# Performance work log

Hardware: AMD Instinct MI355X
Metric: run time of the kernel (lower is better)

The kernel has to match this reference:

```python
import jax, jax.numpy as jnp
import numpy as np

N = 8192
IN_FEATS = 256
D = IN_FEATS // 4  # 64, bottleneck dim
HID = 64           # MLP hidden_dim
K_MAX = 9
K_EC = 20
SLOPE = 0.01       # torch LeakyReLU default


def _leaky(x):
    return jnp.where(x >= 0, x, SLOPE * x)


def _knn_idx(f, k):
    # f: [N, d]; returns [N, k] indices of k nearest (incl. self, dist 0), ascending distance
    sq = jnp.sum(f * f, axis=1)
    dist = sq[:, None] + sq[None, :] - 2.0 * (f @ f.T)  # [N, N]
    _, idx = jax.lax.top_k(-dist, k)
    return idx


def _edge_conv(f, idx, Wt, bt, Wp, bp, W1, b1, W2, b2):
    # f: [N, d]; idx: [N, k] neighbor (src) indices; dst is the row node.
    x_nb = f[idx]                                   # [N, k, d] gather of src feats
    theta = (f[:, None, :] - x_nb) @ Wt.T + bt      # v_sub_u -> theta Linear
    phi = f @ Wp.T + bp                             # [N, d]
    z = phi[:, None, :] + theta                     # [N, k, d]
    # MLP(hidden=64, 2 layers, leaky_relu, activation_first=True)
    z = _leaky(z) @ W1.T + b1
    z = _leaky(z) @ W2.T + b2
    return jnp.max(z, axis=1)                       # max aggregation per dst


def _lin_init(key, out_dim, in_dim):
    k1, k2 = jax.random.split(key)
    bound = 1.0 / np.sqrt(in_dim)
    W = jax.random.uniform(k1, (out_dim, in_dim), jnp.float32, -bound, bound)
    b = jax.random.uniform(k2, (out_dim,), jnp.float32, -bound, bound)
    return W, b


def setup_inputs() -> dict:
    key = jax.random.key(0)
    keys = jax.random.split(key, 12)
    inp = {"feature": jax.random.normal(keys[0], (N, IN_FEATS), jnp.float32)}
    inp["Wb"], inp["bb"] = _lin_init(keys[1], D, IN_FEATS)
    inp["Wt1"], inp["bt1"] = _lin_init(keys[2], D, D)
    inp["Wp1"], inp["bp1"] = _lin_init(keys[3], D, D)
    inp["Wm1a"], inp["bm1a"] = _lin_init(keys[4], HID, D)
    inp["Wm1b"], inp["bm1b"] = _lin_init(keys[5], D, HID)
    inp["Wt2"], inp["bt2"] = _lin_init(keys[6], D, D)
    inp["Wp2"], inp["bp2"] = _lin_init(keys[7], D, D)
    inp["Wm2a"], inp["bm2a"] = _lin_init(keys[8], HID, D)
    inp["Wm2b"], inp["bm2b"] = _lin_init(keys[9], D, HID)
    inp["Wl"], inp["bl"] = _lin_init(keys[10], IN_FEATS, 3 * D)
    return inp


def reference(feature, Wb, bb, Wt1, bt1, Wp1, bp1, Wm1a, bm1a, Wm1b, bm1b,
              Wt2, bt2, Wp2, bp2, Wm2a, bm2a, Wm2b, bm2b, Wl, bl):
    f = feature @ Wb.T + bb                          # bottleneck [N, D]
    # KNN indices are non-differentiable (torch topk indices) -> stop_gradient
    idx40 = _knn_idx(jax.lax.stop_gradient(f), K_EC * 2)  # 40-NN, ascending distance
    idx9 = idx40[:, :K_MAX]
    idx20 = idx40[:, :K_EC]            # dilation 1
    idx20_d2 = idx40[:, ::2]           # dilation 2: every 2nd of 40-NN
    h_max = jnp.max(f[idx9], axis=1)   # copy_u + max over 9-NN
    h1 = _edge_conv(f, idx20, Wt1, bt1, Wp1, bp1, Wm1a, bm1a, Wm1b, bm1b)
    h2 = _edge_conv(f, idx20_d2, Wt2, bt2, Wp2, bp2, Wm2a, bm2a, Wm2b, bm2b)
    h = jnp.concatenate([h1, h2, h_max], axis=1) @ Wl.T + bl
    return h + feature                 # residual
```

## Files before the change

### kernel.cpp

```cpp
#include <hip/hip_runtime.h>
#include <math.h>

#define NPT   8192
#define FIN   256
#define DD    64
#define KSEL  48
#define SSEG  320

#define LEAKY(x) (((x) >= 0.f) ? (x) : 0.01f*(x))

using short8v = __attribute__((ext_vector_type(8))) short;
using f32x4   = __attribute__((ext_vector_type(4))) float;

__device__ inline unsigned short f2bf(float x) {
  union { float f; unsigned u; } v; v.f = x;
  unsigned r = v.u + 0x7fff + ((v.u >> 16) & 1);
  return (unsigned short)(r >> 16);
}
__device__ inline float bf2f(unsigned short h) {
  union { unsigned u; float f; } v; v.u = ((unsigned)h) << 16; return v.f;
}
__device__ inline unsigned key_of(float f) {
  unsigned u = __float_as_uint(f);
  return (u & 0x80000000u) ? ~u : (u | 0x80000000u);
}
__device__ inline float key_inv(unsigned k) {
  unsigned u = (k >> 31) ? (k ^ 0x80000000u) : ~k;
  return __uint_as_float(u);
}

__global__ void k0_prep(const float* __restrict__ Wl, const float* __restrict__ Wb,
                        const float* __restrict__ Wt1, const float* __restrict__ Wp1,
                        const float* __restrict__ Wt2, const float* __restrict__ Wp2,
                        float* __restrict__ WlT, float* __restrict__ WbT,
                        float* __restrict__ WtT1, float* __restrict__ WpT1,
                        float* __restrict__ WtT2, float* __restrict__ WpT2)
{
  const int b = blockIdx.x, t = threadIdx.x;
  if (b < 192) {
    WlT[b*256 + t] = Wl[t*192 + b];
  } else if (b < 256) {
    int j = (b - 192)*4 + (t >> 6), o = t & 63;
    WbT[j*64 + o] = Wb[o*256 + j];
  } else {
    int m = b - 256;
    const float* src = (m==0) ? Wt1 : (m==1) ? Wp1 : (m==2) ? Wt2 : Wp2;
    float*       dst = (m==0) ? WtT1: (m==1) ? WpT1: (m==2) ? WtT2: WpT2;
    #pragma unroll
    for (int i = 0; i < 16; ++i) {
      int idx = t + 256*i, r = idx >> 6, c = idx & 63;
      dst[c*64 + r] = src[r*64 + c];
    }
  }
}

__global__ __launch_bounds__(256) void k1_precompute(
    const float* __restrict__ feature, const float* __restrict__ WbT, const float* __restrict__ bb,
    const float* __restrict__ WtT1, const float* __restrict__ bt1,
    const float* __restrict__ WpT1, const float* __restrict__ bp1,
    const float* __restrict__ WtT2, const float* __restrict__ bt2,
    const float* __restrict__ WpT2, const float* __restrict__ bp2,
    double* __restrict__ f64d, double* __restrict__ sq64,
    float* __restrict__ f32v, float* __restrict__ sqf,
    float* __restrict__ u1, float* __restrict__ c1,
    float* __restrict__ u2, float* __restrict__ c2)
{
  __shared__ float f_s[4*64];
  const int w = threadIdx.x >> 6, l = threadIdx.x & 63;
  const int i = blockIdx.x*4 + w;
  const float* frow = feature + i*FIN;
  double a0 = (double)bb[l], a1 = 0.0, a2 = 0.0, a3 = 0.0;
  #pragma unroll 2
  for (int j = 0; j < FIN; j += 4) {
    float4 fv = *(const float4*)&frow[j];
    a0 += (double)fv.x * (double)WbT[(j+0)*64 + l];
    a1 += (double)fv.y * (double)WbT[(j+1)*64 + l];
    a2 += (double)fv.z * (double)WbT[(j+2)*64 + l];
    a3 += (double)fv.w * (double)WbT[(j+3)*64 + l];
  }
  double facc = (a0 + a1) + (a2 + a3);
  f64d[i*DD + l] = facc;
  float f32 = (float)facc;
  f32v[i*DD + l] = f32;
  double s = facc*facc;
  #pragma unroll
  for (int off = 32; off; off >>= 1) s += __shfl_xor(s, off);
  if (l == 0) { sq64[i] = s; sqf[i] = (float)s; }
  f_s[w*64 + l] = f32;
  float au1 = 0.f, ap1 = 0.f, au2 = 0.f, ap2 = 0.f;
  for (int e = 0; e < DD; ++e) {
    float fe = f_s[w*64 + e];
    au1 += fe * WtT1[e*64 + l];
    ap1 += fe * WpT1[e*64 + l];
    au2 += fe * WtT2[e*64 + l];
    ap2 += fe * WpT2[e*64 + l];
  }
  u1[i*DD+l] = au1;
  c1[i*DD+l] = ap1 + bp1[l] + au1 + bt1[l];
  u2[i*DD+l] = au2;
  c2[i*DD+l] = ap2 + bp2[l] + au2 + bt2[l];
}

__global__ __launch_bounds__(256) void k1b_frag(
    const float* __restrict__ f32v,
    unsigned short* __restrict__ Saf, unsigned short* __restrict__ Sbf)
{
  const int w = threadIdx.x >> 6, l = threadIdx.x & 63;
  const int task = blockIdx.x*4 + w;
  const int tile = task / 6, ks = task % 6;
  const int row  = tile*16 + (l & 15);
  const int inner = (ks & 1)*32 + ((l >> 4) << 3);
  union { unsigned short u[8]; short8v v; } pa, pb;
  #pragma unroll
  for (int j = 0; j < 8; ++j) {
    float x = f32v[row*64 + inner + j];
    unsigned short hi = f2bf(x);
    unsigned short lo = f2bf(x - bf2f(hi));
    pa.u[j] = (ks < 4) ? hi : lo;
    pb.u[j] = (ks < 2) ? hi : ((ks < 4) ? lo : hi);
  }
  size_t off = ((size_t)(tile*6 + ks)*64 + l)*8;
  *(short8v*)&Saf[off] = pa.v;
  *(short8v*)&Sbf[off] = pb.v;
}

__global__ __launch_bounds__(256) void k1c_wfrag(
    const float* __restrict__ Wm1a, const float* __restrict__ Wm1b,
    const float* __restrict__ Wm2a, const float* __restrict__ Wm2b,
    unsigned short* __restrict__ F1a, unsigned short* __restrict__ F1b,
    unsigned short* __restrict__ F2a, unsigned short* __restrict__ F2b)
{
  const int w = threadIdx.x >> 6, l = threadIdx.x & 63;
  const int task = blockIdx.x*4 + w;
  const int which = task / 24, rem = task % 24;
  const int nt = rem / 6, ks = rem % 6;
  const float* W = (which==0) ? Wm1a : (which==1) ? Wm1b : (which==2) ? Wm2a : Wm2b;
  unsigned short* F = (which==0) ? F1a : (which==1) ? F1b : (which==2) ? F2a : F2b;
  const int row = nt*16 + (l & 15);
  const int inner = (ks & 1)*32 + ((l >> 4) << 3);
  union { unsigned short u[8]; short8v v; } p;
  #pragma unroll
  for (int j = 0; j < 8; ++j) {
    float x = W[row*64 + inner + j];
    unsigned short hi = f2bf(x);
    unsigned short lo = f2bf(x - bf2f(hi));
    p.u[j] = (ks < 2) ? hi : ((ks < 4) ? lo : hi);
  }
  *(short8v*)&F[((size_t)(nt*6 + ks)*64 + l)*8] = p.v;
}

#define MFMA_PAIR6(ACC, AF, BF)                                                  \
  ACC = __builtin_amdgcn_mfma_f32_16x16x32_bf16(AF[0], BF[0], ACC, 0, 0, 0);     \
  ACC = __builtin_amdgcn_mfma_f32_16x16x32_bf16(AF[1], BF[1], ACC, 0, 0, 0);     \
  ACC = __builtin_amdgcn_mfma_f32_16x16x32_bf16(AF[0], BF[2], ACC, 0, 0, 0);     \
  ACC = __builtin_amdgcn_mfma_f32_16x16x32_bf16(AF[1], BF[3], ACC, 0, 0, 0);     \
  ACC = __builtin_amdgcn_mfma_f32_16x16x32_bf16(AF[2], BF[0], ACC, 0, 0, 0);     \
  ACC = __builtin_amdgcn_mfma_f32_16x16x32_bf16(AF[3], BF[1], ACC, 0, 0, 0);

__global__ __launch_bounds__(512) void k2a_sample(
    const unsigned short* __restrict__ Saf,
    const unsigned short* __restrict__ Sbf,
    const float* __restrict__ sqf,
    float* __restrict__ sampD)
{
  const int t = threadIdx.x, w = t >> 6, l = t & 63;
  const int qb = blockIdx.x >> 1, sh = blockIdx.x & 1;
  const int qbase = qb * 32;
  short8v afr[2][4];
  #pragma unroll
  for (int mt = 0; mt < 2; ++mt) {
    const size_t b = (size_t)(qb*2 + mt)*6;
    afr[mt][0] = *(const short8v*)&Saf[((b+0)*64 + l)*8];
    afr[mt][1] = *(const short8v*)&Saf[((b+1)*64 + l)*8];
    afr[mt][2] = *(const short8v*)&Saf[((b+4)*64 + l)*8];
    afr[mt][3] = *(const short8v*)&Saf[((b+5)*64 + l)*8];
  }
  const int ncol = w*16 + (l & 15);
  for (int sl = 0; sl < 4; ++sl) {
    const int s = sh*4 + sl;
    const int cb = s*8;
    const int jbase = cb*128;
    short8v bfr[4];
    {
      const size_t b = (size_t)(cb*8 + w)*6;
      #pragma unroll
      for (int k = 0; k < 4; ++k)
        bfr[k] = *(const short8v*)&Sbf[((b+k)*64 + l)*8];
    }
    const float sc = sqf[jbase + ncol];
    f32x4 acc0 = {0.f,0.f,0.f,0.f}, acc1 = {0.f,0.f,0.f,0.f};
    MFMA_PAIR6(acc0, afr[0], bfr);
    MFMA_PAIR6(acc1, afr[1], bfr);
    #pragma unroll
    for (int r = 0; r < 4; ++r) {
      const int q0 = qbase + 0*16 + (l >> 4)*4 + r;
      const int q1 = qbase + 1*16 + (l >> 4)*4 + r;
      sampD[(size_t)q0*1024 + s*128 + ncol] = sc - 2.0f*acc0[r];
      sampD[(size_t)q1*1024 + s*128 + ncol] = sc - 2.0f*acc1[r];
    }
  }
}

__global__ __launch_bounds__(256) void k2t_threshold(
    const float* __restrict__ sampD, float* __restrict__ Tq)
{
  const int w = threadIdx.x >> 6, l = threadIdx.x & 63;
  const int q = blockIdx.x*4 + w;
  unsigned ku[16];
  #pragma unroll
  for (int k = 0; k < 16; ++k)
    ku[k] = key_of(sampD[(size_t)q*1024 + k*64 + l]);
  unsigned prefix = 0; int need = 41;
  for (int b = 31; b >= 0; --b) {
    unsigned p2 = prefix << 1;
    int c = 0;
    #pragma unroll
    for (int k = 0; k < 16; ++k) c += ((ku[k] >> b) == p2);
    #pragma unroll
    for (int off = 32; off; off >>= 1) c += __shfl_xor(c, off);
    if (c >= need) prefix = p2; else { prefix = p2 | 1u; need -= c; }
  }
  if (l == 0) Tq[q] = key_inv(prefix);
}

__global__ __launch_bounds__(512) void k2f_filter(
    const unsigned short* __restrict__ Saf,
    const unsigned short* __restrict__ Sbf,
    const float* __restrict__ sqf,
    const float* __restrict__ Tq,
    int* __restrict__ cnt_g,
    float* __restrict__ survD, int* __restrict__ survI)
{
  __shared__ int cnt_sh[32];
  const int t = threadIdx.x, w = t >> 6, l = t & 63;
  const int qb = blockIdx.x >> 1, half = blockIdx.x & 1;
  const int qbase = qb * 32;
  if (t < 32) cnt_sh[t] = 0;
  short8v afr[2][4];
  float Tr[2][4]; int qloc[2][4];
  #pragma unroll
  for (int mt = 0; mt < 2; ++mt) {
    const size_t b = (size_t)(qb*2 + mt)*6;
    afr[mt][0] = *(const short8v*)&Saf[((b+0)*64 + l)*8];
    afr[mt][1] = *(const short8v*)&Saf[((b+1)*64 + l)*8];
    afr[mt][2] = *(const short8v*)&Saf[((b+4)*64 + l)*8];
    afr[mt][3] = *(const short8v*)&Saf[((b+5)*64 + l)*8];
    #pragma unroll
    for (int r = 0; r < 4; ++r) {
      qloc[mt][r] = mt*16 + (l >> 4)*4 + r;
      Tr[mt][r] = Tq[qbase + qloc[mt][r]];
    }
  }
  short8v bfr[4];
  {
    const size_t b = (size_t)(half*256 + w)*6;
    #pragma unroll
    for (int k = 0; k < 4; ++k)
      bfr[k] = *(const short8v*)&Sbf[((b+k)*64 + l)*8];
  }
  const int ncol = w*16 + (l & 15);
  __syncthreads();
  for (int cb = 0; cb < 32; ++cb) {
    const int jbase = half*4096 + cb*128;
    const float sc = sqf[jbase + ncol];
    f32x4 acc0 = {0.f,0.f,0.f,0.f}, acc1 = {0.f,0.f,0.f,0.f};
    MFMA_PAIR6(acc0, afr[0], bfr);
    MFMA_PAIR6(acc1, afr[1], bfr);
    if (cb < 31) {
      const size_t b = (size_t)(half*256 + (cb+1)*8 + w)*6;
      #pragma unroll
      for (int k = 0; k < 4; ++k)
        bfr[k] = *(const short8v*)&Sbf[((b+k)*64 + l)*8];
    }
    const int j = jbase + ncol;
    #pragma unroll
    for (int r = 0; r < 4; ++r) {
      float d0 = sc - 2.0f*acc0[r];
      if (d0 < Tr[0][r]) {
        int slot = atomicAdd(&cnt_sh[qloc[0][r]], 1);
        if (slot < SSEG) {
          size_t base = ((size_t)(qbase + qloc[0][r])*2 + half)*SSEG + slot;
          survD[base] = d0; survI[base] = j;
        }
      }
      float d1 = sc - 2.0f*acc1[r];
      if (d1 < Tr[1][r]) {
        int slot = atomicAdd(&cnt_sh[qloc[1][r]], 1);
        if (slot < SSEG) {
          size_t base = ((size_t)(qbase + qloc[1][r])*2 + half)*SSEG + slot;
          survD[base] = d1; survI[base] = j;
        }
      }
    }
  }
  __syncthreads();
  if (t < 32) cnt_g[(qbase + t)*2 + half] = cnt_sh[t];
}

__global__ __launch_bounds__(256) void k2s_select(
    const float* __restrict__ survD, const int* __restrict__ survI,
    const int* __restrict__ cnt_g, int* __restrict__ idx48)
{
  const int w = threadIdx.x >> 6, l = threadIdx.x & 63;
  const int node = blockIdx.x*4 + w;
  const int c0 = min(cnt_g[node*2 + 0], SSEG);
  const int c1 = min(cnt_g[node*2 + 1], SSEG);
  unsigned ku[10]; int iv[10];
  #pragma unroll
  for (int k = 0; k < 10; ++k) {
    int e = k*64 + l;
    int seg = (e >= SSEG);
    int off = e - seg*SSEG;
    bool v = off < (seg ? c1 : c0);
    size_t base = ((size_t)node*2 + seg)*SSEG + off;
    float d = v ? survD[base] : 0.f;
    iv[k] = v ? survI[base] : 0;
    ku[k] = v ? key_of(d) : 0xFFFFFFFFu;
  }
  unsigned prefix = 0; int need = KSEL;
  for (int b = 31; b >= 0; --b) {
    unsigned p2 = prefix << 1;
    int c = 0;
    #pragma unroll
    for (int k = 0; k < 10; ++k) c += ((ku[k] >> b) == p2);
    #pragma unroll
    for (int off = 32; off; off >>= 1) c += __shfl_xor(c, off);
    if (c >= need) prefix = p2; else { prefix = p2 | 1u; need -= c; }
  }
  const unsigned long long below = (1ull << l) - 1ull;
  int base = 0;
  #pragma unroll
  for (int k = 0; k < 10; ++k) {
    unsigned long long blt = __ballot(ku[k] < prefix);
    if (ku[k] < prefix) {
      int pos = base + __popcll(blt & below);
      idx48[(size_t)node*KSEL + pos] = iv[k];
    }
    base += __popcll(blt);
  }
  #pragma unroll
  for (int k = 0; k < 10; ++k) {
    unsigned long long beq = __ballot(ku[k] == prefix);
    if (ku[k] == prefix) {
      int pos = base + __popcll(beq & below);
      if (pos < KSEL) idx48[(size_t)node*KSEL + pos] = iv[k];
    }
    base += __popcll(beq);
  }
}

__global__ __launch_bounds__(256) void k2r_rerank(
    const double* __restrict__ f64d, const double* __restrict__ sq64,
    const int* __restrict__ idx48, int* __restrict__ idx40)
{
  __shared__ double part[KSEL][4];
  __shared__ double dist_sh[KSEL];
  __shared__ int    cand_sh[KSEL];
  const int t = threadIdx.x;
  const int node = blockIdx.x;
  if (t < KSEL) cand_sh[t] = idx48[(size_t)node*KSEL + t];
  __syncthreads();
  if (t < 192) {
    int c = t >> 2, qt = t & 3;
    int cand = cand_sh[c];
    const double* fi = f64d + (size_t)node*DD + qt*16;
    const double* fc = f64d + (size_t)cand*DD + qt*16;
    double a0 = 0.0, a1 = 0.0;
    #pragma unroll
    for (int d = 0; d < 16; d += 2) { a0 += fi[d]*fc[d]; a1 += fi[d+1]*fc[d+1]; }
    part[c][qt] = a0 + a1;
  }
  __syncthreads();
  if (t < KSEL) {
    int cand = cand_sh[t];
    dist_sh[t] = sq64[node] + sq64[cand]
               - 2.0*(part[t][0] + part[t][1] + part[t][2] + part[t][3]);
  }
  __syncthreads();
  if (t < KSEL) {
    double dm = dist_sh[t]; int cand = cand_sh[t];
    int rank = 0;
    for (int j = 0; j < KSEL; ++j) {
      double dj = dist_sh[j];
      int    ij = cand_sh[j];
      rank += (dj < dm) || (dj == dm && ij < cand);
    }
    if (rank < 40) idx40[(size_t)node*40 + rank] = cand;
  }
}

#define MFMA6(ACC, AF, W0, W1, W2, W3)                                          \
  ACC = __builtin_amdgcn_mfma_f32_16x16x32_bf16(AF[0], W0, ACC, 0, 0, 0);       \
  ACC = __builtin_amdgcn_mfma_f32_16x16x32_bf16(AF[1], W1, ACC, 0, 0, 0);       \
  ACC = __builtin_amdgcn_mfma_f32_16x16x32_bf16(AF[0], W2, ACC, 0, 0, 0);       \
  ACC = __builtin_amdgcn_mfma_f32_16x16x32_bf16(AF[1], W3, ACC, 0, 0, 0);       \
  ACC = __builtin_amdgcn_mfma_f32_16x16x32_bf16(AF[2], W0, ACC, 0, 0, 0);       \
  ACC = __builtin_amdgcn_mfma_f32_16x16x32_bf16(AF[3], W1, ACC, 0, 0, 0);

__global__ __launch_bounds__(256) void k3_edgeconv(
    const float* __restrict__ f32v,
    const float* __restrict__ u1, const float* __restrict__ c1,
    const float* __restrict__ u2, const float* __restrict__ c2,
    const unsigned short* __restrict__ F1a, const unsigned short* __restrict__ F1b,
    const unsigned short* __restrict__ F2a, const unsigned short* __restrict__ F2b,
    const float* __restrict__ bm1a, const float* __restrict__ bm1b,
    const float* __restrict__ bm2a, const float* __restrict__ bm2b,
    const int* __restrict__ idx40, float* __restrict__ hout)
{
  __shared__ __align__(16) unsigned au32[32*66];
  __shared__ float red_s[2*64];
  __shared__ int idx_sh[40];
  const int t = threadIdx.x, i = blockIdx.x;
  const int w = t >> 6, l = t & 63;
  const int mt = w >> 1;
  const int nb0 = (w & 1)*2;
  const int row16 = l & 15;
  const int q8 = (l >> 4) << 3;
  if (t < 40) idx_sh[t] = idx40[i*40 + t];
  __syncthreads();

  for (int conv = 0; conv < 2; ++conv) {
    const float* u_g = conv ? u2 : u1;
    const float* c_g = conv ? c2 : c1;
    const unsigned short* WfA = conv ? F2a : F1a;
    const unsigned short* WfB = conv ? F2b : F1b;
    const float* bav = conv ? bm2a : bm1a;
    const float* bbv = conv ? bm2b : bm1b;

    const int row = mt*16 + row16;
    const bool valid = row < 20;
    const int nb = valid ? idx_sh[conv ? 2*row : row] : idx_sh[0];
    short8v afr[4];
    {
      const float* up = u_g + (size_t)nb*DD;
      const float* cp = c_g + (size_t)i*DD;
      float4 ua = *(const float4*)&up[q8];
      float4 ub = *(const float4*)&up[q8 + 4];
      float4 uc = *(const float4*)&up[32 + q8];
      float4 ud = *(const float4*)&up[32 + q8 + 4];
      float4 ca = *(const float4*)&cp[q8];
      float4 cb2 = *(const float4*)&cp[q8 + 4];
      float4 cc = *(const float4*)&cp[32 + q8];
      float4 cd = *(const float4*)&cp[32 + q8 + 4];
      float z0[8], z1[8];
      z0[0]=ca.x-ua.x;  z0[1]=ca.y-ua.y;  z0[2]=ca.z-ua.z;  z0[3]=ca.w-ua.w;
      z0[4]=cb2.x-ub.x; z0[5]=cb2.y-ub.y; z0[6]=cb2.z-ub.z; z0[7]=cb2.w-ub.w;
      z1[0]=cc.x-uc.x;  z1[1]=cc.y-uc.y;  z1[2]=cc.z-uc.z;  z1[3]=cc.w-uc.w;
      z1[4]=cd.x-ud.x;  z1[5]=cd.y-ud.y;  z1[6]=cd.z-ud.z;  z1[7]=cd.w-ud.w;
      union { unsigned short us[8]; short8v v; } fh0, fh1, fl0, fl1;
      #pragma unroll
      for (int j = 0; j < 8; ++j) {
        float x0 = valid ? LEAKY(z0[j]) : 0.f;
        float x1 = valid ? LEAKY(z1[j]) : 0.f;
        unsigned short h0 = f2bf(x0);
        unsigned short h1 = f2bf(x1);
        fh0.us[j] = h0; fl0.us[j] = f2bf(x0 - bf2f(h0));
        fh1.us[j] = h1; fl1.us[j] = f2bf(x1 - bf2f(h1));
      }
      afr[0] = fh0.v; afr[1] = fh1.v; afr[2] = fl0.v; afr[3] = fl1.v;
    }
    f32x4 acc0 = {0.f,0.f,0.f,0.f}, acc1 = {0.f,0.f,0.f,0.f};
    {
      const unsigned short* p0 = WfA + ((size_t)(nb0+0)*6*64)*8;
      const unsigned short* p1 = WfA + ((size_t)(nb0+1)*6*64)*8;
      short8v w00 = *(const short8v*)&p0[(0*64+l)*8];
      short8v w01 = *(const short8v*)&p0[(1*64+l)*8];
      short8v w02 = *(const short8v*)&p0[(2*64+l)*8];
      short8v w03 = *(const short8v*)&p0[(3*64+l)*8];
      short8v w10 = *(const short8v*)&p1[(0*64+l)*8];
      short8v w11 = *(const short8v*)&p1[(1*64+l)*8];
      short8v w12 = *(const short8v*)&p1[(2*64+l)*8];
      short8v w13 = *(const short8v*)&p1[(3*64+l)*8];
      MFMA6(acc0, afr, w00, w01, w02, w03);
      MFMA6(acc1, afr, w10, w11, w12, w13);
    }
    {
      const int c0 = (nb0+0)*16 + row16, c1i = (nb0+1)*16 + row16;
      const float ba0 = bav[c0], ba1 = bav[c1i];
      #pragma unroll
      for (int r = 0; r < 4; ++r) {
        const int arow = mt*16 + (l >> 4)*4 + r;
        float v0 = acc0[r] + ba0; v0 = LEAKY(v0);
        float v1 = acc1[r] + ba1; v1 = LEAKY(v1);
        unsigned short h0 = f2bf(v0), h1 = f2bf(v1);
        unsigned lo0 = f2bf(v0 - bf2f(h0));
        unsigned lo1 = f2bf(v1 - bf2f(h1));
        au32[arow*66 + c0]  = (unsigned)h0 | (lo0 << 16);
        au32[arow*66 + c1i] = (unsigned)h1 | (lo1 << 16);
      }
    }
    __syncthreads();
    short8v bfr[4];
    {
      const int base = (mt*16 + row16)*66 + q8;
      union { unsigned u[4]; short8v v; } bh0, bh1, bl0, bl1;
      #pragma unroll
      for (int p = 0; p < 4; ++p) {
        uint2 lo2 = *(const uint2*)&au32[base + 2*p];
        uint2 hi2 = *(const uint2*)&au32[base + 32 + 2*p];
        bh0.u[p] = (lo2.x & 0xFFFFu) | (lo2.y << 16);
        bl0.u[p] = (lo2.x >> 16)     | (lo2.y & 0xFFFF0000u);
        bh1.u[p] = (hi2.x & 0xFFFFu) | (hi2.y << 16);
        bl1.u[p] = (hi2.x >> 16)     | (hi2.y & 0xFFFF0000u);
      }
      bfr[0] = bh0.v; bfr[1] = bh1.v; bfr[2] = bl0.v; bfr[3] = bl1.v;
    }
    f32x4 bacc0 = {0.f,0.f,0.f,0.f}, bacc1 = {0.f,0.f,0.f,0.f};
    {
      const unsigned short* p0 = WfB + ((size_t)(nb0+0)*6*64)*8;
      const unsigned short* p1 = WfB + ((size_t)(nb0+1)*6*64)*8;
      short8v w00 = *(const short8v*)&p0[(0*64+l)*8];
      short8v w01 = *(const short8v*)&p0[(1*64+l)*8];
      short8v w02 = *(const short8v*)&p0[(2*64+l)*8];
      short8v w03 = *(const short8v*)&p0[(3*64+l)*8];
      short8v w10 = *(const short8v*)&p1[(0*64+l)*8];
      short8v w11 = *(const short8v*)&p1[(1*64+l)*8];
      short8v w12 = *(const short8v*)&p1[(2*64+l)*8];
      short8v w13 = *(const short8v*)&p1[(3*64+l)*8];
      MFMA6(bacc0, bfr, w00, w01, w02, w03);
      MFMA6(bacc1, bfr, w10, w11, w12, w13);
    }
    {
      const int c0 = (nb0+0)*16 + row16, c1i = (nb0+1)*16 + row16;
      const float bb0 = bbv[c0], bb1 = bbv[c1i];
      float m0 = -__builtin_inff(), m1 = -__builtin_inff();
      #pragma unroll
      for (int r = 0; r < 4; ++r) {
        const int arow = mt*16 + (l >> 4)*4 + r;
        if (arow < 20) {
          m0 = fmaxf(m0, bacc0[r] + bb0);
          m1 = fmaxf(m1, bacc1[r] + bb1);
        }
      }
      m0 = fmaxf(m0, __shfl_xor(m0, 16)); m0 = fmaxf(m0, __shfl_xor(m0, 32));
      m1 = fmaxf(m1, __shfl_xor(m1, 16)); m1 = fmaxf(m1, __shfl_xor(m1, 32));
      if ((l >> 4) == 0) {
        red_s[mt*64 + c0]  = m0;
        red_s[mt*64 + c1i] = m1;
      }
    }
    __syncthreads();
    if (t < 64) hout[i*192 + conv*64 + t] = fmaxf(red_s[t], red_s[64 + t]);
    __syncthreads();
  }
  if (t < 64) {
    float m = -__builtin_inff();
    #pragma unroll
    for (int k = 0; k < 9; ++k) m = fmaxf(m, f32v[idx_sh[k]*DD + t]);
    hout[i*192 + 128 + t] = m;
  }
}

__global__ __launch_bounds__(256) void k4_final(
    const float* __restrict__ hbuf, const float* __restrict__ WlT,
    const float* __restrict__ bl, const float* __restrict__ feature,
    float* __restrict__ out)
{
  __shared__ __align__(16) float h_sh[16*192];
  const int t = threadIdx.x;
  const int nbase = blockIdx.x * 16;
  #pragma unroll
  for (int r = 0; r < 3; ++r) {
    int flat = t + 256*r;
    int n = flat / 48, j4 = flat % 48;
    *(float4*)&h_sh[n*192 + 4*j4] = *(const float4*)&hbuf[(nbase+n)*192 + 4*j4];
  }
  __syncthreads();
  float acc[16];
  #pragma unroll
  for (int n = 0; n < 16; ++n) acc[n] = 0.f;
  for (int j4 = 0; j4 < 48; ++j4) {
    float w0 = WlT[(4*j4+0)*256 + t];
    float w1 = WlT[(4*j4+1)*256 + t];
    float w2 = WlT[(4*j4+2)*256 + t];
    float w3 = WlT[(4*j4+3)*256 + t];
    #pragma unroll
    for (int n = 0; n < 16; ++n) {
      float4 hv = *(const float4*)&h_sh[n*192 + 4*j4];
      acc[n] += hv.x*w0 + hv.y*w1 + hv.z*w2 + hv.w*w3;
    }
  }
  float blv = bl[t];
  #pragma unroll
  for (int n = 0; n < 16; ++n)
    out[(nbase+n)*256 + t] = acc[n] + blv + feature[(nbase+n)*256 + t];
}

extern "C" void kernel_launch(void* const* d_in, const int* in_sizes, int n_in,
                              void* d_out, int out_size, void* d_ws, size_t ws_size,
                              hipStream_t stream) {
  const float* feature = (const float*)d_in[0];
  const float* Wb   = (const float*)d_in[1];
  const float* bb   = (const float*)d_in[2];
  const float* Wt1  = (const float*)d_in[3];
  const float* bt1  = (const float*)d_in[4];
  const float* Wp1  = (const float*)d_in[5];
  const float* bp1  = (const float*)d_in[6];
  const float* Wm1a = (const float*)d_in[7];
  const float* bm1a = (const float*)d_in[8];
  const float* Wm1b = (const float*)d_in[9];
  const float* bm1b = (const float*)d_in[10];
  const float* Wt2  = (const float*)d_in[11];
  const float* bt2  = (const float*)d_in[12];
  const float* Wp2  = (const float*)d_in[13];
  const float* bp2  = (const float*)d_in[14];
  const float* Wm2a = (const float*)d_in[15];
  const float* bm2a = (const float*)d_in[16];
  const float* Wm2b = (const float*)d_in[17];
  const float* bm2b = (const float*)d_in[18];
  const float* Wl   = (const float*)d_in[19];
  const float* bl   = (const float*)d_in[20];
  float* out = (float*)d_out;

  char* ws = (char*)d_ws;
  double* f64d = (double*)(ws + 0);
  double* sq64 = (double*)(ws + 4194304);
  float*  f32v = (float*)(ws + 4259840);
  float*  sqf  = (float*)(ws + 6356992);
  float*  u1   = (float*)(ws + 6389760);
  float*  c1   = (float*)(ws + 8486912);
  float*  u2   = (float*)(ws + 10584064);
  float*  c2   = (float*)(ws + 12681216);
  int*    idx48= (int*)(ws + 14778368);
  int*    idx40= (int*)(ws + 16351232);
  float*  hbuf = (float*)(ws + 17661952);
  float*  WlT  = (float*)(ws + 23953408);
  unsigned short* Saf = (unsigned short*)(ws + 24150016);
  unsigned short* Sbf = (unsigned short*)(ws + 27295744);
  float*  WbT  = (float*)(ws + 30441472);
  float*  WtT1 = (float*)(ws + 30507008);
  float*  WpT1 = (float*)(ws + 30523392);
  float*  WtT2 = (float*)(ws + 30539776);
  float*  WpT2 = (float*)(ws + 30556160);
  unsigned short* F1a = (unsigned short*)(ws + 30572544);
  unsigned short* F1b = (unsigned short*)(ws + 30597120);
  unsigned short* F2a = (unsigned short*)(ws + 30621696);
  unsigned short* F2b = (unsigned short*)(ws + 30646272);
  float*  Tq   = (float*)(ws + 30670848);
  int*    cnt_g= (int*)(ws + 30703616);
  float*  survD= (float*)(ws + 30769152);
  int*    survI= (int*)(ws + 51740672);
  float*  sampD= (float*)(ws + 30769152);

  hipLaunchKernelGGL(k0_prep, dim3(260), dim3(256), 0, stream,
                     Wl, Wb, Wt1, Wp1, Wt2, Wp2, WlT, WbT, WtT1, WpT1, WtT2, WpT2);
  hipLaunchKernelGGL(k1c_wfrag, dim3(24), dim3(256), 0, stream,
                     Wm1a, Wm1b, Wm2a, Wm2b, F1a, F1b, F2a, F2b);
  hipLaunchKernelGGL(k1_precompute, dim3(2048), dim3(256), 0, stream,
                     feature, WbT, bb, WtT1, bt1, WpT1, bp1, WtT2, bt2, WpT2, bp2,
                     f64d, sq64, f32v, sqf, u1, c1, u2, c2);
  hipLaunchKernelGGL(k1b_frag, dim3(768), dim3(256), 0, stream, f32v, Saf, Sbf);
  hipLaunchKernelGGL(k2a_sample, dim3(512), dim3(512), 0, stream, Saf, Sbf, sqf, sampD);
  hipLaunchKernelGGL(k2t_threshold, dim3(2048), dim3(256), 0, stream, sampD, Tq);
  hipLaunchKernelGGL(k2f_filter, dim3(512), dim3(512), 0, stream,
                     Saf, Sbf, sqf, Tq, cnt_g, survD, survI);
  hipLaunchKernelGGL(k2s_select, dim3(2048), dim3(256), 0, stream, survD, survI, cnt_g, idx48);
  hipLaunchKernelGGL(k2r_rerank, dim3(8192), dim3(256), 0, stream, f64d, sq64, idx48, idx40);
  hipLaunchKernelGGL(k3_edgeconv, dim3(8192), dim3(256), 0, stream,
                     f32v, u1, c1, u2, c2, F1a, F1b, F2a, F2b,
                     bm1a, bm1b, bm2a, bm2b, idx40, hbuf);
  hipLaunchKernelGGL(k4_final, dim3(512), dim3(256), 0, stream, hbuf, WlT, bl, feature, out);
}
```

Baseline: 432.6 us.

## Drop split-bf16 MLP in edgeconv and process two nodes per block

The edgeconv MLP previously used a hi/lo bf16 split (six MFMAs per output tile) to approximate fp32 precision. It now uses plain bf16 operands (two MFMAs per tile), and each wave computes all four output column tiles. Each block now handles two destination nodes, halving the grid. The goal is to cut MFMA and conversion work and block launch overhead, at the cost of lower numerical precision in the MLP, which could threaten tolerance.

New measurement: 396.7 us. 1.09x faster.

```diff
diff --git a/kernel.cpp b/kernel.cpp
--- a/kernel.cpp
+++ b/kernel.cpp
@@ -389,14 +389,6 @@
   }
 }
 
-#define MFMA6(ACC, AF, W0, W1, W2, W3)                                          \
-  ACC = __builtin_amdgcn_mfma_f32_16x16x32_bf16(AF[0], W0, ACC, 0, 0, 0);       \
-  ACC = __builtin_amdgcn_mfma_f32_16x16x32_bf16(AF[1], W1, ACC, 0, 0, 0);       \
-  ACC = __builtin_amdgcn_mfma_f32_16x16x32_bf16(AF[0], W2, ACC, 0, 0, 0);       \
-  ACC = __builtin_amdgcn_mfma_f32_16x16x32_bf16(AF[1], W3, ACC, 0, 0, 0);       \
-  ACC = __builtin_amdgcn_mfma_f32_16x16x32_bf16(AF[2], W0, ACC, 0, 0, 0);       \
-  ACC = __builtin_amdgcn_mfma_f32_16x16x32_bf16(AF[3], W1, ACC, 0, 0, 0);
-
 __global__ __launch_bounds__(256) void k3_edgeconv(
     const float* __restrict__ f32v,
     const float* __restrict__ u1, const float* __restrict__ c1,
@@ -407,16 +399,16 @@
     const float* __restrict__ bm2a, const float* __restrict__ bm2b,
     const int* __restrict__ idx40, float* __restrict__ hout)
 {
-  __shared__ __align__(16) unsigned au32[32*66];
-  __shared__ float red_s[2*64];
-  __shared__ int idx_sh[40];
-  const int t = threadIdx.x, i = blockIdx.x;
+  __shared__ unsigned short au16[2][32*72];
+  __shared__ float red_s[2][2][64];
+  __shared__ int idx_sh[80];
+  const int t = threadIdx.x;
   const int w = t >> 6, l = t & 63;
-  const int mt = w >> 1;
-  const int nb0 = (w & 1)*2;
+  const int sub = w >> 1, mt = w & 1;
+  const int i = blockIdx.x*2 + sub;
   const int row16 = l & 15;
   const int q8 = (l >> 4) << 3;
-  if (t < 40) idx_sh[t] = idx40[i*40 + t];
+  if (t < 80) idx_sh[t] = idx40[(size_t)(blockIdx.x*2 + (t >= 40))*40 + (t >= 40 ? t - 40 : t)];
   __syncthreads();
 
   for (int conv = 0; conv < 2; ++conv) {
@@ -429,8 +421,8 @@
 
     const int row = mt*16 + row16;
     const bool valid = row < 20;
-    const int nb = valid ? idx_sh[conv ? 2*row : row] : idx_sh[0];
-    short8v afr[4];
+    const int nb = valid ? idx_sh[sub*40 + (conv ? 2*row : row)] : idx_sh[sub*40];
+    short8v fr0, fr1;
     {
       const float* up = u_g + (size_t)nb*DD;
       const float* cp = c_g + (size_t)i*DD;
@@ -439,115 +431,88 @@
       float4 uc = *(const float4*)&up[32 + q8];
       float4 ud = *(const float4*)&up[32 + q8 + 4];
       float4 ca = *(const float4*)&cp[q8];
-      float4 cb2 = *(const float4*)&cp[q8 + 4];
+      float4 cb = *(const float4*)&cp[q8 + 4];
       float4 cc = *(const float4*)&cp[32 + q8];
       float4 cd = *(const float4*)&cp[32 + q8 + 4];
-      float z0[8], z1[8];
-      z0[0]=ca.x-ua.x;  z0[1]=ca.y-ua.y;  z0[2]=ca.z-ua.z;  z0[3]=ca.w-ua.w;
-      z0[4]=cb2.x-ub.x; z0[5]=cb2.y-ub.y; z0[6]=cb2.z-ub.z; z0[7]=cb2.w-ub.w;
-      z1[0]=cc.x-uc.x;  z1[1]=cc.y-uc.y;  z1[2]=cc.z-uc.z;  z1[3]=cc.w-uc.w;
-      z1[4]=cd.x-ud.x;  z1[5]=cd.y-ud.y;  z1[6]=cd.z-ud.z;  z1[7]=cd.w-ud.w;
-      union { unsigned short us[8]; short8v v; } fh0, fh1, fl0, fl1;
+      float z0[8] = {ca.x-ua.x, ca.y-ua.y, ca.z-ua.z, ca.w-ua.w,
+                     cb.x-ub.x, cb.y-ub.y, cb.z-ub.z, cb.w-ub.w};
+      float z1[8] = {cc.x-uc.x, cc.y-uc.y, cc.z-uc.z, cc.w-uc.w,
+                     cd.x-ud.x, cd.y-ud.y, cd.z-ud.z, cd.w-ud.w};
+      union { unsigned short us[8]; short8v v; } h0, h1;
       #pragma unroll
       for (int j = 0; j < 8; ++j) {
         float x0 = valid ? LEAKY(z0[j]) : 0.f;
         float x1 = valid ? LEAKY(z1[j]) : 0.f;
-        unsigned short h0 = f2bf(x0);
-        unsigned short h1 = f2bf(x1);
-        fh0.us[j] = h0; fl0.us[j] = f2bf(x0 - bf2f(h0));
-        fh1.us[j] = h1; fl1.us[j] = f2bf(x1 - bf2f(h1));
+        h0.us[j] = f2bf(x0);
+        h1.us[j] = f2bf(x1);
       }
-      afr[0] = fh0.v; afr[1] = fh1.v; afr[2] = fl0.v; afr[3] = fl1.v;
-    }
-    f32x4 acc0 = {0.f,0.f,0.f,0.f}, acc1 = {0.f,0.f,0.f,0.f};
-    {
-      const unsigned short* p0 = WfA + ((size_t)(nb0+0)*6*64)*8;
-      const unsigned short* p1 = WfA + ((size_t)(nb0+1)*6*64)*8;
-      short8v w00 = *(const short8v*)&p0[(0*64+l)*8];
-      short8v w01 = *(const short8v*)&p0[(1*64+l)*8];
-      short8v w02 = *(const short8v*)&p0[(2*64+l)*8];
-      short8v w03 = *(const short8v*)&p0[(3*64+l)*8];
-      short8v w10 = *(const short8v*)&p1[(0*64+l)*8];
-      short8v w11 = *(const short8v*)&p1[(1*64+l)*8];
-      short8v w12 = *(const short8v*)&p1[(2*64+l)*8];
-      short8v w13 = *(const short8v*)&p1[(3*64+l)*8];
-      MFMA6(acc0, afr, w00, w01, w02, w03);
-      MFMA6(acc1, afr, w10, w11, w12, w13);
-    }
-    {
-      const int c0 = (nb0+0)*16 + row16, c1i = (nb0+1)*16 + row16;
-      const float ba0 = bav[c0], ba1 = bav[c1i];
+      fr0 = h0.v; fr1 = h1.v;
+    }
+    f32x4 acc[4] = {{0,0,0,0},{0,0,0,0},{0,0,0,0},{0,0,0,0}};
+    #pragma unroll
+    for (int nt = 0; nt < 4; ++nt) {
+      const unsigned short* p = WfA + (size_t)nt*6*64*8;
+      short8v w0 = *(const short8v*)&p[(0*64 + l)*8];
+      short8v w1 = *(const short8v*)&p[(1*64 + l)*8];
+      acc[nt] = __builtin_amdgcn_mfma_f32_16x16x32_bf16(fr0, w0, acc[nt], 0, 0, 0);
+      acc[nt] = __builtin_amdgcn_mfma_f32_16x16x32_bf16(fr1, w1, acc[nt], 0, 0, 0);
+    }
+    #pragma unroll
+    for (int nt = 0; nt < 4; ++nt) {
+      const int col = nt*16 + row16;
+      const float ba = bav[col];
       #pragma unroll
       for (int r = 0; r < 4; ++r) {
         const int arow = mt*16 + (l >> 4)*4 + r;
-        float v0 = acc0[r] + ba0; v0 = LEAKY(v0);
-        float v1 = acc1[r] + ba1; v1 = LEAKY(v1);
-        unsigned short h0 = f2bf(v0), h1 = f2bf(v1);
-        unsigned lo0 = f2bf(v0 - bf2f(h0));
-        unsigned lo1 = f2bf(v1 - bf2f(h1));
-        au32[arow*66 + c0]  = (unsigned)h0 | (lo0 << 16);
-        au32[arow*66 + c1i] = (unsigned)h1 | (lo1 << 16);
+        float v = acc[nt][r] + ba; v = LEAKY(v);
+        au16[sub][arow*72 + col] = f2bf(v);
       }
     }
     __syncthreads();
-    short8v bfr[4];
+    short8v g0, g1;
     {
-      const int base = (mt*16 + row16)*66 + q8;
-      union { unsigned u[4]; short8v v; } bh0, bh1, bl0, bl1;
-      #pragma unroll
-      for (int p = 0; p < 4; ++p) {
-        uint2 lo2 = *(const uint2*)&au32[base + 2*p];
-        uint2 hi2 = *(const uint2*)&au32[base + 32 + 2*p];
-        bh0.u[p] = (lo2.x & 0xFFFFu) | (lo2.y << 16);
-        bl0.u[p] = (lo2.x >> 16)     | (lo2.y & 0xFFFF0000u);
-        bh1.u[p] = (hi2.x & 0xFFFFu) | (hi2.y << 16);
-        bl1.u[p] = (hi2.x >> 16)     | (hi2.y & 0xFFFF0000u);
-      }
-      bfr[0] = bh0.v; bfr[1] = bh1.v; bfr[2] = bl0.v; bfr[3] = bl1.v;
-    }
-    f32x4 bacc0 = {0.f,0.f,0.f,0.f}, bacc1 = {0.f,0.f,0.f,0.f};
-    {
-      const unsigned short* p0 = WfB + ((size_t)(nb0+0)*6*64)*8;
-      const unsigned short* p1 = WfB + ((size_t)(nb0+1)*6*64)*8;
-      short8v w00 = *(const short8v*)&p0[(0*64+l)*8];
-      short8v w01 = *(const short8v*)&p0[(1*64+l)*8];
-      short8v w02 = *(const short8v*)&p0[(2*64+l)*8];
-      short8v w03 = *(const short8v*)&p0[(3*64+l)*8];
-      short8v w10 = *(const short8v*)&p1[(0*64+l)*8];
-      short8v w11 = *(const short8v*)&p1[(1*64+l)*8];
-      short8v w12 = *(const short8v*)&p1[(2*64+l)*8];
-      short8v w13 = *(const short8v*)&p1[(3*64+l)*8];
-      MFMA6(bacc0, bfr, w00, w01, w02, w03);
-      MFMA6(bacc1, bfr, w10, w11, w12, w13);
-    }
-    {
-      const int c0 = (nb0+0)*16 + row16, c1i = (nb0+1)*16 + row16;
-      const float bb0 = bbv[c0], bb1 = bbv[c1i];
-      float m0 = -__builtin_inff(), m1 = -__builtin_inff();
+      const unsigned short* base = &au16[sub][(mt*16 + row16)*72 + q8];
+      g0 = *(const short8v*)&base[0];
+      g1 = *(const short8v*)&base[32];
+    }
+    f32x4 bacc[4] = {{0,0,0,0},{0,0,0,0},{0,0,0,0},{0,0,0,0}};
+    #pragma unroll
+    for (int nt = 0; nt < 4; ++nt) {
+      const unsigned short* p = WfB + (size_t)nt*6*64*8;
+      short8v w0 = *(const short8v*)&p[(0*64 + l)*8];
+      short8v w1 = *(const short8v*)&p[(1*64 + l)*8];
+      bacc[nt] = __builtin_amdgcn_mfma_f32_16x16x32_bf16(g0, w0, bacc[nt], 0, 0, 0);
+      bacc[nt] = __builtin_amdgcn_mfma_f32_16x16x32_bf16(g1, w1, bacc[nt], 0, 0, 0);
+    }
+    #pragma unroll
+    for (int nt = 0; nt < 4; ++nt) {
+      const int col = nt*16 + row16;
+      const float bb2 = bbv[col];
+      float m = -__builtin_inff();
       #pragma unroll
       for (int r = 0; r < 4; ++r) {
         const int arow = mt*16 + (l >> 4)*4 + r;
-        if (arow < 20) {
-          m0 = fmaxf(m0, bacc0[r] + bb0);
-          m1 = fmaxf(m1, bacc1[r] + bb1);
-        }
+        if (arow < 20) m = fmaxf(m, bacc[nt][r] + bb2);
       }
-      m0 = fmaxf(m0, __shfl_xor(m0, 16)); m0 = fmaxf(m0, __shfl_xor(m0, 32));
-      m1 = fmaxf(m1, __shfl_xor(m1, 16)); m1 = fmaxf(m1, __shfl_xor(m1, 32));
-      if ((l >> 4) == 0) {
-        red_s[mt*64 + c0]  = m0;
-        red_s[mt*64 + c1i] = m1;
-      }
+      m = fmaxf(m, __shfl_xor(m, 16));
+      m = fmaxf(m, __shfl_xor(m, 32));
+      if ((l >> 4) == 0) red_s[sub][mt][col] = m;
     }
     __syncthreads();
-    if (t < 64) hout[i*192 + conv*64 + t] = fmaxf(red_s[t], red_s[64 + t]);
+    if (t < 128) {
+      int s2 = t >> 6, col = t & 63;
+      hout[(size_t)(blockIdx.x*2 + s2)*192 + conv*64 + col] =
+          fmaxf(red_s[s2][0][col], red_s[s2][1][col]);
+    }
     __syncthreads();
   }
-  if (t < 64) {
+  if (t < 128) {
+    int s2 = t >> 6, col = t & 63;
     float m = -__builtin_inff();
     #pragma unroll
-    for (int k = 0; k < 9; ++k) m = fmaxf(m, f32v[idx_sh[k]*DD + t]);
-    hout[i*192 + 128 + t] = m;
+    for (int k = 0; k < 9; ++k)
+      m = fmaxf(m, f32v[(size_t)idx_sh[s2*40 + k]*DD + col]);
+    hout[(size_t)(blockIdx.x*2 + s2)*192 + 128 + col] = m;
   }
 }
 
@@ -656,7 +621,7 @@
                      Saf, Sbf, sqf, Tq, cnt_g, survD, survI);
   hipLaunchKernelGGL(k2s_select, dim3(2048), dim3(256), 0, stream, survD, survI, cnt_g, idx48);
   hipLaunchKernelGGL(k2r_rerank, dim3(8192), dim3(256), 0, stream, f64d, sq64, idx48, idx40);
-  hipLaunchKernelGGL(k3_edgeconv, dim3(8192), dim3(256), 0, stream,
+  hipLaunchKernelGGL(k3_edgeconv, dim3(4096), dim3(256), 0, stream,
                      f32v, u1, c1, u2, c2, F1a, F1b, F2a, F2b,
                      bm1a, bm1b, bm2a, bm2b, idx40, hbuf);
   hipLaunchKernelGGL(k4_final, dim3(512), dim3(256), 0, stream, hbuf, WlT, bl, feature, out);
```
